# Kernel optimization log

Measured on AMD Instinct MI355X. Metric: run time of the kernel, lower is better.

## Reference

```python
import jax, jax.numpy as jnp
import numpy as np

ALIBI_SLOPES = jnp.array([0.6299605249, 0.396850263, 0.25, 0.1574901312,
                          0.0992125657, 0.0625, 0.0393725328, 0.0248031414,
                          0.015625, 0.0098431332, 0.0062007854, 0.00390625],
                         dtype=jnp.float32)
H, D = 12, 64
SCALE = D ** (-0.5)


def setup_inputs() -> dict:
    key = jax.random.key(0)
    ks = jax.random.split(key, 9)
    B, S, E = 4, 2048, 768
    s = 0.02
    return {
        "x": jax.random.normal(ks[0], (B, S, E), dtype=jnp.float32),
        "Wq": jax.random.normal(ks[1], (E, E), dtype=jnp.float32) * s,
        "bq": jnp.zeros((E,), dtype=jnp.float32),
        "Wk": jax.random.normal(ks[2], (E, E), dtype=jnp.float32) * s,
        "bk": jnp.zeros((E,), dtype=jnp.float32),
        "Wv": jax.random.normal(ks[3], (E, E), dtype=jnp.float32) * s,
        "bv": jnp.zeros((E,), dtype=jnp.float32),
        "Wo": jax.random.normal(ks[4], (E, E), dtype=jnp.float32) * s,
        "bo": jnp.zeros((E,), dtype=jnp.float32),
    }


def reference(x, Wq, bq, Wk, bk, Wv, bv, Wo, bo):
    B, S, E = x.shape
    # projections (weights stored input-major: y = x @ W + b)
    q = (x @ Wq + bq).reshape(B, S, H, D).transpose(0, 2, 1, 3)  # [B,H,S,D]
    k = (x @ Wk + bk).reshape(B, S, H, D).transpose(0, 2, 1, 3)
    v = (x @ Wv + bv).reshape(B, S, H, D).transpose(0, 2, 1, 3)

    scores = jnp.einsum('bhqd,bhkd->bhqk', q, k) * SCALE  # [B,H,S,S]

    pos = jnp.arange(S, dtype=jnp.float32)
    a = ALIBI_SLOPES[:, None] * pos[None, :]          # [H,S]
    alibi = a[:, :, None] - a[:, None, :]             # [H,S,S]
    scores = scores + alibi[None]

    causal = jnp.triu(jnp.ones((S, S), dtype=bool), k=1)  # True above diag
    scores = jnp.where(causal[None, None], -jnp.inf, scores)

    attn = jax.nn.softmax(scores, axis=-1)
    o = jnp.einsum('bhqk,bhkd->bhqd', attn, v)  # [B,H,S,D]

    # Faithful to original: view of contiguous (B,H,S,D) buffer as (B,S,E)
    # (head-major flatten, reproducing the original module's reshape).
    o = o.reshape(B, S, E)
    return o @ Wo + bo
```

## Files before the change

### kernel.cpp

```cpp
#include <hip/hip_runtime.h>
#include <hip/hip_bf16.h>
#include <cstdint>
#include <cstddef>

#define B_ 4
#define S_ 2048
#define E_ 768
#define H_ 12
#define D_ 64

typedef __bf16 bf16x8 __attribute__((ext_vector_type(8)));
typedef float f32x4 __attribute__((ext_vector_type(4)));

__constant__ float c_slopes[12] = {
    0.6299605249f, 0.396850263f, 0.25f, 0.1574901312f,
    0.0992125657f, 0.0625f, 0.0393725328f, 0.0248031414f,
    0.015625f, 0.0098431332f, 0.0062007854f, 0.00390625f};

__device__ __forceinline__ unsigned short f2bf_u(float f) {
    unsigned u = __builtin_bit_cast(unsigned, f);
    u += 0x7fffu + ((u >> 16) & 1u);
    return (unsigned short)(u >> 16);
}
__device__ __forceinline__ __bf16 f2bf(float f) {
    unsigned short s = f2bf_u(f);
    return __builtin_bit_cast(__bf16, s);
}

__device__ __forceinline__ void gload_lds16(const void* g, void* l) {
    __builtin_amdgcn_global_load_lds(
        (const __attribute__((address_space(1))) unsigned int*)g,
        (__attribute__((address_space(3))) unsigned int*)l, 16, 0, 0);
}

__global__ __launch_bounds__(256) void cvt_x(const float* __restrict__ src,
                                             __bf16* __restrict__ dst) {
    int i = (blockIdx.x * 256 + threadIdx.x) * 4;
    float4 v = *(const float4*)(src + i);
    ushort4 o;
    o.x = f2bf_u(v.x); o.y = f2bf_u(v.y); o.z = f2bf_u(v.z); o.w = f2bf_u(v.w);
    *(ushort4*)((unsigned short*)dst + i) = o;
}

__global__ __launch_bounds__(256) void wtrans(const float* __restrict__ W0,
                                              const float* __restrict__ W1,
                                              const float* __restrict__ W2,
                                              const float* __restrict__ W3,
                                              __bf16* __restrict__ Wt) {
    const float* W = blockIdx.z == 0 ? W0 : blockIdx.z == 1 ? W1
                   : blockIdx.z == 2 ? W2 : W3;
    __bf16* out = Wt + (size_t)blockIdx.z * E_ * E_;
    __shared__ alignas(16) __bf16 ts[64 * 72];
    const int t = threadIdx.x;
    const int k0 = blockIdx.y * 64, n0 = blockIdx.x * 64;
#pragma unroll
    for (int i = 0; i < 4; i++) {
        int idx = i * 256 + t;
        int row = idx >> 4, c4 = idx & 15;
        float4 v = *(const float4*)(W + (size_t)(k0 + row) * E_ + n0 + c4 * 4);
        ts[(c4 * 4 + 0) * 72 + row] = f2bf(v.x);
        ts[(c4 * 4 + 1) * 72 + row] = f2bf(v.y);
        ts[(c4 * 4 + 2) * 72 + row] = f2bf(v.z);
        ts[(c4 * 4 + 3) * 72 + row] = f2bf(v.w);
    }
    __syncthreads();
#pragma unroll
    for (int i = 0; i < 2; i++) {
        int idx = i * 256 + t;
        int r = idx >> 3, c8 = idx & 7;
        *(uint4*)((unsigned short*)out + (size_t)(n0 + r) * E_ + k0 + c8 * 8) =
            *(const uint4*)((const unsigned short*)ts + r * 72 + c8 * 8);
    }
}

template <bool PERM>
__global__ __launch_bounds__(256) void gemm_bf(
    const __bf16* __restrict__ A, const __bf16* __restrict__ WtAll,
    const float* __restrict__ b0, const float* __restrict__ b1,
    const float* __restrict__ b2,
    float* __restrict__ outF, __bf16* __restrict__ outB_base) {
    constexpr int Kd = E_, N = E_;
    __shared__ alignas(16) __bf16 Asm[128 * 32];
    __shared__ alignas(16) __bf16 Bsm[128 * 32];

    const int t = threadIdx.x;
    const int w = t >> 6, lane = t & 63;
    const int qm = lane & 15, quad = lane >> 4;
    const int m0 = blockIdx.y * 128, n0 = blockIdx.x * 128;
    const int wm = (w >> 1) * 64, wn = (w & 1) * 64;
    const int z = blockIdx.z;
    const __bf16* Wt = WtAll + (size_t)z * Kd * N;
    const float* bias = PERM ? (z == 0 ? b0 : z == 1 ? b1 : b2) : b0;
    __bf16* outB = PERM ? outB_base + (size_t)z * ((size_t)B_ * S_ * E_) : nullptr;

    float bvv[4];
#pragma unroll
    for (int j = 0; j < 4; j++) bvv[j] = bias[n0 + wn + j * 16 + qm];

    const int crow = lane >> 2;
    const int ccol = lane & 3;

    f32x4 acc[4][4] = {};

    for (int k0 = 0; k0 < Kd; k0 += 32) {
#pragma unroll
        for (int cc = 0; cc < 2; cc++) {
            int chunk = w * 2 + cc;
            int row = chunk * 16 + crow;
            gload_lds16((const unsigned short*)A + (size_t)(m0 + row) * Kd + k0 + ccol * 8,
                        Asm + chunk * 512);
            gload_lds16((const unsigned short*)Wt + (size_t)(n0 + row) * Kd + k0 + ccol * 8,
                        Bsm + chunk * 512);
        }
        __syncthreads();

        bf16x8 af[4], bg[4];
#pragma unroll
        for (int i = 0; i < 4; i++)
            af[i] = *(const bf16x8*)(Asm + (wm + i * 16 + qm) * 32 + quad * 8);
#pragma unroll
        for (int j = 0; j < 4; j++)
            bg[j] = *(const bf16x8*)(Bsm + (wn + j * 16 + qm) * 32 + quad * 8);
#pragma unroll
        for (int i = 0; i < 4; i++)
#pragma unroll
            for (int j = 0; j < 4; j++)
                acc[i][j] = __builtin_amdgcn_mfma_f32_16x16x32_bf16(
                    af[i], bg[j], acc[i][j], 0, 0, 0);
        __syncthreads();
    }

#pragma unroll
    for (int i = 0; i < 4; i++) {
#pragma unroll
        for (int j = 0; j < 4; j++) {
            int col = n0 + wn + j * 16 + qm;
            int rowb = m0 + wm + i * 16 + quad * 4;
            if (PERM && z == 2) {
                int b = rowb >> 11, s = rowb & (S_ - 1);
                int h = col >> 6, d = col & (D_ - 1);
                unsigned short pk4[4];
#pragma unroll
                for (int r = 0; r < 4; r++) pk4[r] = f2bf_u(acc[i][j][r] + bvv[j]);
                uint2 pv;
                pv.x = (unsigned)pk4[0] | ((unsigned)pk4[1] << 16);
                pv.y = (unsigned)pk4[2] | ((unsigned)pk4[3] << 16);
                *(uint2*)((unsigned short*)outB +
                          ((size_t)(b * H_ + h) * D_ + d) * S_ + s) = pv;
            } else {
#pragma unroll
                for (int r = 0; r < 4; r++) {
                    int row = rowb + r;
                    float val = acc[i][j][r] + bvv[j];
                    if (PERM) {
                        int b = row >> 11, s = row & (S_ - 1);
                        int h = col >> 6, d = col & (D_ - 1);
                        outB[(((size_t)(b * H_ + h)) * S_ + s) * D_ + d] = f2bf(val);
                    } else {
                        outF[(size_t)row * N + col] = val;
                    }
                }
            }
        }
    }
}

__global__ __launch_bounds__(256, 6) void attn_k(
    const __bf16* __restrict__ Q, const __bf16* __restrict__ K,
    const __bf16* __restrict__ Vt, __bf16* __restrict__ O) {
    __shared__ alignas(16) __bf16 Ksm[2][64 * 32];
    __shared__ alignas(16) __bf16 Vsm[2][64 * 32];
    __shared__ alignas(16) __bf16 Psm[4 * 16 * 64];

    const int t = threadIdx.x;
    const int w = t >> 6, lane = t & 63;
    const int qm = lane & 15, quad = lane >> 4;
    const int L = blockIdx.x;
    const int r = L & 7;
    const int m = (L >> 3) & 31;
    const int s = L >> 8;
    const int bh = r * 6 + s;
    const int qt = (m + s * 5 + (s >> 1)) & 31;
    const float c2 = c_slopes[bh % H_] * 1.44269504f;
    const size_t base = (size_t)bh * S_ * D_;

    const int bb = qt * 64 + w * 16;
    const __bf16* qp = Q + base + (size_t)(bb + qm) * D_ + quad * 8;
    bf16x8 qf0 = *(const bf16x8*)qp;
    bf16x8 qf1 = *(const bf16x8*)(qp + 32);

    f32x4 oacc[4] = {};
    float lsum = 0.f;
    char* Pb = (char*)Psm + w * 2048;

    const int srow = lane >> 2;
    const int sq = (lane & 3) ^ ((lane >> 3) & 3);
    const unsigned short* Kg = (const unsigned short*)K + base +
                               (size_t)(16 * w + srow) * D_ + sq * 8;
    const unsigned short* Vg = (const unsigned short*)Vt + base +
                               (size_t)(16 * w + srow) * S_ + sq * 8;

    const int cq = (quad ^ ((qm >> 1) & 3)) * 8;
    const int pf = (qm & 7) << 4;

    for (int kt = 0; kt <= qt; kt++) {
#pragma unroll
        for (int h = 0; h < 2; h++) {
            gload_lds16(Kg + (size_t)(kt * 64) * D_ + 32 * h, Ksm[h] + w * 512);
            gload_lds16(Vg + kt * 64 + 32 * h, Vsm[h] + w * 512);
        }
        __syncthreads();

        bf16x8 ak[4][2], bv[4][2];
#pragma unroll
        for (int i = 0; i < 4; i++) {
            ak[i][0] = *(const bf16x8*)(Ksm[0] + (16 * i + qm) * 32 + cq);
            ak[i][1] = *(const bf16x8*)(Ksm[1] + (16 * i + qm) * 32 + cq);
        }
#pragma unroll
        for (int jd = 0; jd < 4; jd++) {
            bv[jd][0] = *(const bf16x8*)(Vsm[0] + (16 * jd + qm) * 32 + cq);
            bv[jd][1] = *(const bf16x8*)(Vsm[1] + (16 * jd + qm) * 32 + cq);
        }

        f32x4 st[4];
#pragma unroll
        for (int i = 0; i < 4; i++) {
            f32x4 zz = {0.f, 0.f, 0.f, 0.f};
            zz = __builtin_amdgcn_mfma_f32_16x16x32_bf16(ak[i][0], qf0, zz, 0, 0, 0);
            zz = __builtin_amdgcn_mfma_f32_16x16x32_bf16(ak[i][1], qf1, zz, 0, 0, 0);
            st[i] = zz;
        }

        const int qi = bb + qm;
        const bool nomask = (kt * 64 + 63) <= bb;
        float ls = 0.f;
        unsigned pk[4][2];
#pragma unroll
        for (int i = 0; i < 4; i++) {
            float bi = -c2 * (float)(kt * 64 + 16 * i + 4 * quad);
            float p[4];
#pragma unroll
            for (int rr = 0; rr < 4; rr++) {
                float tt = st[i][rr] * 0.18033688f + (bi - c2 * (float)rr);
                float pp = __builtin_amdgcn_exp2f(tt);
                if (!nomask) {
                    int key = kt * 64 + 16 * i + 4 * quad + rr;
                    pp = (key > qi) ? 0.f : pp;
                }
                ls += pp;
                p[rr] = pp;
            }
            unsigned u0 = __builtin_bit_cast(unsigned, p[0]) + 0x8000u;
            unsigned u1 = __builtin_bit_cast(unsigned, p[1]) + 0x8000u;
            unsigned u2 = __builtin_bit_cast(unsigned, p[2]) + 0x8000u;
            unsigned u3 = __builtin_bit_cast(unsigned, p[3]) + 0x8000u;
            pk[i][0] = __builtin_amdgcn_perm(u1, u0, 0x07060302u);
            pk[i][1] = __builtin_amdgcn_perm(u3, u2, 0x07060302u);
        }
        lsum += ls;

#pragma unroll
        for (int i = 0; i < 4; i++) {
            uint2 pv; pv.x = pk[i][0]; pv.y = pk[i][1];
            *(uint2*)(Pb + qm * 128 + ((32 * i + 8 * quad) ^ pf)) = pv;
        }

        bf16x8 ap0 = *(const bf16x8*)(Pb + qm * 128 + ((quad * 16) ^ pf));
        bf16x8 ap1 = *(const bf16x8*)(Pb + qm * 128 + ((64 + quad * 16) ^ pf));
#pragma unroll
        for (int jd = 0; jd < 4; jd++) {
            oacc[jd] = __builtin_amdgcn_mfma_f32_16x16x32_bf16(
                ap0, bv[jd][0], oacc[jd], 0, 0, 0);
            oacc[jd] = __builtin_amdgcn_mfma_f32_16x16x32_bf16(
                ap1, bv[jd][1], oacc[jd], 0, 0, 0);
        }

        __syncthreads();
    }

    float lf = lsum;
    lf += __shfl_xor(lf, 16);
    lf += __shfl_xor(lf, 32);
#pragma unroll
    for (int rr = 0; rr < 4; rr++) {
        float lr = __shfl(lf, 4 * quad + rr);
        float inv = 1.0f / lr;
        int qrow = bb + 4 * quad + rr;
#pragma unroll
        for (int jd = 0; jd < 4; jd++)
            O[base + (size_t)qrow * D_ + 16 * jd + qm] =
                f2bf(oacc[jd][rr] * inv);
    }
}

extern "C" void kernel_launch(void* const* d_in, const int* in_sizes, int n_in,
                              void* d_out, int out_size, void* d_ws, size_t ws_size,
                              hipStream_t stream) {
    (void)in_sizes; (void)n_in; (void)out_size; (void)ws_size;
    const float* x  = (const float*)d_in[0];
    const float* Wq = (const float*)d_in[1];
    const float* bq = (const float*)d_in[2];
    const float* Wk = (const float*)d_in[3];
    const float* bk = (const float*)d_in[4];
    const float* Wv = (const float*)d_in[5];
    const float* bv = (const float*)d_in[6];
    const float* Wo = (const float*)d_in[7];
    const float* bo = (const float*)d_in[8];
    float* out = (float*)d_out;

    const size_t n = (size_t)B_ * H_ * S_ * D_;
    __bf16* xb  = (__bf16*)d_ws;
    __bf16* Qb  = xb + n;
    __bf16* Kb  = xb + 2 * n;
    __bf16* Vtb = xb + 3 * n;
    __bf16* Wt  = xb + 4 * n;
    __bf16* Ob  = Qb;

    cvt_x<<<6144, 256, 0, stream>>>(x, xb);
    wtrans<<<dim3(12, 12, 4), 256, 0, stream>>>(Wq, Wk, Wv, Wo, Wt);
    gemm_bf<true><<<dim3(6, 64, 3), 256, 0, stream>>>(
        xb, Wt, bq, bk, bv, nullptr, Qb);
    attn_k<<<1536, 256, 0, stream>>>(Qb, Kb, Vtb, Ob);
    gemm_bf<false><<<dim3(6, 64, 1), 256, 0, stream>>>(
        Ob, Wt + 3 * (size_t)E_ * E_, bo, nullptr, nullptr, out, nullptr);
}
```

Baseline: 237.7 us.

## Fuse Q/K/V projections into one GEMM sharing the activation tile

Adds a dedicated QKV GEMM kernel in which each block loads one 128-row tile of x and multiplies it against three 64-column weight tiles (Q, K, V) at once. The old path launched a batched GEMM where each z-slice reloaded the same activation tile. The aim is to cut repeated activation loads from global memory and LDS. In exchange each wave computes a 32x64 tile per matrix, which needs more accumulator registers, and the kernel runs at a lower occupancy bound. The generic GEMM loses its permuted-output branch.

```diff
diff --git a/kernel.cpp b/kernel.cpp
--- a/kernel.cpp
+++ b/kernel.cpp
@@ -73,6 +73,106 @@
     }
 }
 
+__global__ __launch_bounds__(256, 3) void qkv_gemm(
+    const __bf16* __restrict__ A, const __bf16* __restrict__ WtAll,
+    const float* __restrict__ b0, const float* __restrict__ b1,
+    const float* __restrict__ b2, __bf16* __restrict__ Qb,
+    __bf16* __restrict__ Kb, __bf16* __restrict__ Vtb) {
+    constexpr int Kd = E_;
+    __shared__ alignas(16) __bf16 Asm[128 * 32];
+    __shared__ alignas(16) __bf16 Bsm[3][64 * 32];
+
+    const int t = threadIdx.x;
+    const int w = t >> 6, lane = t & 63;
+    const int qm = lane & 15, quad = lane >> 4;
+    const int m0 = blockIdx.y * 128, n0 = blockIdx.x * 64;
+    const int wm = w * 32;
+
+    float bvv[3][4];
+    const float* bs[3] = {b0, b1, b2};
+#pragma unroll
+    for (int z = 0; z < 3; z++)
+#pragma unroll
+        for (int j = 0; j < 4; j++) bvv[z][j] = bs[z][n0 + j * 16 + qm];
+
+    const int crow = lane >> 2;
+    const int ccol = lane & 3;
+
+    f32x4 acc[3][2][4] = {};
+
+    for (int k0 = 0; k0 < Kd; k0 += 32) {
+#pragma unroll
+        for (int cc = 0; cc < 2; cc++) {
+            int chunk = w * 2 + cc;
+            gload_lds16((const unsigned short*)A +
+                            (size_t)(m0 + chunk * 16 + crow) * Kd + k0 + ccol * 8,
+                        Asm + chunk * 512);
+        }
+#pragma unroll
+        for (int e = 0; e < 3; e++) {
+            int g = w * 3 + e;
+            int z = g >> 2, cz = g & 3;
+            gload_lds16((const unsigned short*)WtAll + (size_t)z * Kd * E_ +
+                            (size_t)(n0 + cz * 16 + crow) * Kd + k0 + ccol * 8,
+                        Bsm[z] + cz * 512);
+        }
+        __syncthreads();
+
+        bf16x8 af[2];
+#pragma unroll
+        for (int i = 0; i < 2; i++)
+            af[i] = *(const bf16x8*)(Asm + (wm + i * 16 + qm) * 32 + quad * 8);
+#pragma unroll
+        for (int z = 0; z < 3; z++) {
+            bf16x8 bg[4];
+#pragma unroll
+            for (int j = 0; j < 4; j++)
+                bg[j] = *(const bf16x8*)(Bsm[z] + (j * 16 + qm) * 32 + quad * 8);
+#pragma unroll
+            for (int i = 0; i < 2; i++)
+#pragma unroll
+                for (int j = 0; j < 4; j++)
+                    acc[z][i][j] = __builtin_amdgcn_mfma_f32_16x16x32_bf16(
+                        af[i], bg[j], acc[z][i][j], 0, 0, 0);
+        }
+        __syncthreads();
+    }
+
+#pragma unroll
+    for (int z = 0; z < 3; z++) {
+        __bf16* out = z == 0 ? Qb : z == 1 ? Kb : Vtb;
+#pragma unroll
+        for (int i = 0; i < 2; i++) {
+#pragma unroll
+            for (int j = 0; j < 4; j++) {
+                int col = n0 + j * 16 + qm;
+                int rowb = m0 + wm + i * 16 + quad * 4;
+                int h = col >> 6, d = col & (D_ - 1);
+                if (z == 2) {
+                    int b = rowb >> 11, s = rowb & (S_ - 1);
+                    unsigned short pk4[4];
+#pragma unroll
+                    for (int r = 0; r < 4; r++)
+                        pk4[r] = f2bf_u(acc[z][i][j][r] + bvv[z][j]);
+                    uint2 pv;
+                    pv.x = (unsigned)pk4[0] | ((unsigned)pk4[1] << 16);
+                    pv.y = (unsigned)pk4[2] | ((unsigned)pk4[3] << 16);
+                    *(uint2*)((unsigned short*)out +
+                              ((size_t)(b * H_ + h) * D_ + d) * S_ + s) = pv;
+                } else {
+#pragma unroll
+                    for (int r = 0; r < 4; r++) {
+                        int row = rowb + r;
+                        int b = row >> 11, s = row & (S_ - 1);
+                        out[(((size_t)(b * H_ + h)) * S_ + s) * D_ + d] =
+                            f2bf(acc[z][i][j][r] + bvv[z][j]);
+                    }
+                }
+            }
+        }
+    }
+}
+
 template <bool PERM>
 __global__ __launch_bounds__(256) void gemm_bf(
     const __bf16* __restrict__ A, const __bf16* __restrict__ WtAll,
@@ -136,30 +236,11 @@
         for (int j = 0; j < 4; j++) {
             int col = n0 + wn + j * 16 + qm;
             int rowb = m0 + wm + i * 16 + quad * 4;
-            if (PERM && z == 2) {
-                int b = rowb >> 11, s = rowb & (S_ - 1);
-                int h = col >> 6, d = col & (D_ - 1);
-                unsigned short pk4[4];
-#pragma unroll
-                for (int r = 0; r < 4; r++) pk4[r] = f2bf_u(acc[i][j][r] + bvv[j]);
-                uint2 pv;
-                pv.x = (unsigned)pk4[0] | ((unsigned)pk4[1] << 16);
-                pv.y = (unsigned)pk4[2] | ((unsigned)pk4[3] << 16);
-                *(uint2*)((unsigned short*)outB +
-                          ((size_t)(b * H_ + h) * D_ + d) * S_ + s) = pv;
-            } else {
-#pragma unroll
-                for (int r = 0; r < 4; r++) {
-                    int row = rowb + r;
-                    float val = acc[i][j][r] + bvv[j];
-                    if (PERM) {
-                        int b = row >> 11, s = row & (S_ - 1);
-                        int h = col >> 6, d = col & (D_ - 1);
-                        outB[(((size_t)(b * H_ + h)) * S_ + s) * D_ + d] = f2bf(val);
-                    } else {
-                        outF[(size_t)row * N + col] = val;
-                    }
-                }
+#pragma unroll
+            for (int r = 0; r < 4; r++) {
+                int row = rowb + r;
+                float val = acc[i][j][r] + bvv[j];
+                outF[(size_t)row * N + col] = val;
             }
         }
     }
@@ -319,8 +400,8 @@
 
     cvt_x<<<6144, 256, 0, stream>>>(x, xb);
     wtrans<<<dim3(12, 12, 4), 256, 0, stream>>>(Wq, Wk, Wv, Wo, Wt);
-    gemm_bf<true><<<dim3(6, 64, 3), 256, 0, stream>>>(
-        xb, Wt, bq, bk, bv, nullptr, Qb);
+    qkv_gemm<<<dim3(12, 64), 256, 0, stream>>>(
+        xb, Wt, bq, bk, bv, Qb, Kb, Vtb);
     attn_k<<<1536, 256, 0, stream>>>(Qb, Kb, Vtb, Ob);
     gemm_bf<false><<<dim3(6, 64, 1), 256, 0, stream>>>(
         Ob, Wt + 3 * (size_t)E_ * E_, bo, nullptr, nullptr, out, nullptr);
```

After: 218.5 us. 1.09x faster.
